# Performance work log

Hardware: AMD Instinct MI355X
Metric: run time of the kernel (lower is better)

Reference implementation:

```python
import jax, jax.numpy as jnp
import numpy as np

N_MLP = 1024  # number of independent tiny MLPs
D_IN, D_HID, D_OUT = 2, 4, 1
B = 16384


def setup_inputs() -> dict:
    key = jax.random.key(0)
    k = jax.random.split(key, 6)
    x = jax.random.normal(k[0], (B, N_MLP), dtype=jnp.float32)
    x_aug = jax.random.normal(k[1], (B, N_MLP), dtype=jnp.float32)
    # Stacked per-MLP parameters (nn.Linear default init ~ U(-1/sqrt(fan_in), 1/sqrt(fan_in)))
    s1 = 1.0 / np.sqrt(D_IN)
    s2 = 1.0 / np.sqrt(D_HID)
    W1 = jax.random.uniform(k[2], (N_MLP, D_HID, D_IN), jnp.float32, -s1, s1)
    b1 = jax.random.uniform(k[3], (N_MLP, D_HID), jnp.float32, -s1, s1)
    W2 = jax.random.uniform(k[4], (N_MLP, D_OUT, D_HID), jnp.float32, -s2, s2)
    b2 = jax.random.uniform(k[5], (N_MLP, D_OUT), jnp.float32, -s2, s2)
    return {"x": x, "x_aug": x_aug, "W1": W1, "b1": b1, "W2": W2, "b2": b2}


def reference(x, x_aug, W1, b1, W2, b2):
    # data: [B, N, 2] — pair (original, augmented) per feature
    data = jnp.stack([x, x_aug], axis=-1)
    # batched tiny GEMM across the N_MLP axis: [B,N,2] x [N,4,2] -> [B,N,4]
    h = jax.nn.relu(jnp.einsum('bne,nhe->bnh', data, W1) + b1)
    # [B,N,4] x [N,1,4] -> [B,N,1]
    o = jnp.einsum('bnh,noh->bno', h, W2) + b2
    # concat over dim1 of per-MLP [B,1] outputs == squeeze -> [B,N]; mean over N -> [B]
    return jnp.mean(o[..., 0], axis=1)
```

## Files before the change

kernel.cpp:

```cpp
#include <hip/hip_runtime.h>


constexpr int N_MLP = 1024;
constexpr int BATCH = 16384;
constexpr int ROWS = 16;
constexpr int NTHREADS = 256;
constexpr int QN = 256;
constexpr int NQ = N_MLP / QN;

typedef __attribute__((address_space(3))) void lds_void;
typedef const __attribute__((address_space(1))) void gbl_void;

__global__ __launch_bounds__(256)
void zero_out_kernel(float* __restrict__ out) {
    out[blockIdx.x * 256 + threadIdx.x] = 0.0f;
}

__global__ __launch_bounds__(NTHREADS)
void disc_mlp_kernel(const float* __restrict__ x,
                     const float* __restrict__ xa,
                     const float* __restrict__ W1,
                     const float* __restrict__ b1,
                     const float* __restrict__ W2,
                     const float* __restrict__ b2,
                     float* __restrict__ out)
{
    __shared__ float xbuf[ROWS * QN];
    __shared__ float abuf[ROWS * QN];
    __shared__ float red[NTHREADS / 64][ROWS];

    const int t    = threadIdx.x;
    const int lane = t & 63;
    const int wave = t >> 6;
    const int q  = blockIdx.x & (NQ - 1);
    const int rb = blockIdx.x >> 2;
    const int b0 = rb * ROWS;
    const int n  = q * QN + t;

    const float4 p0 = reinterpret_cast<const float4*>(W1)[(size_t)n * 2];
    const float4 p1 = reinterpret_cast<const float4*>(W1)[(size_t)n * 2 + 1];
    const float4 bb = reinterpret_cast<const float4*>(b1)[n];
    const float4 ww = reinterpret_cast<const float4*>(W2)[n];
    const float  b2r = b2[n];

    const float* gx = x  + (size_t)b0 * N_MLP + q * QN;
    const float* ga = xa + (size_t)b0 * N_MLP + q * QN;
#pragma unroll
    for (int i = 0; i < ROWS / 4; ++i) {
        const int r = wave * (ROWS / 4) + i;
        const float* srcx = gx + (size_t)r * N_MLP + lane * 4;
        const float* srca = ga + (size_t)r * N_MLP + lane * 4;
        __builtin_amdgcn_global_load_lds((gbl_void*)srcx,
                                         (lds_void*)&xbuf[r * QN + lane * 4],
                                         16, 0, 0);
        __builtin_amdgcn_global_load_lds((gbl_void*)srca,
                                         (lds_void*)&abuf[r * QN + lane * 4],
                                         16, 0, 0);
    }
    __syncthreads();

    const float A[4]   = {p0.x, p0.z, p1.x, p1.z};
    const float C[4]   = {p0.y, p0.w, p1.y, p1.w};
    const float B1r[4] = {bb.x, bb.y, bb.z, bb.w};
    const float V[4]   = {ww.x, ww.y, ww.z, ww.w};

    float acc[ROWS];
#pragma unroll
    for (int r = 0; r < ROWS; ++r) {
        const float xe  = xbuf[r * QN + t];
        const float xae = abuf[r * QN + t];
        float s = b2r;
#pragma unroll
        for (int j = 0; j < 4; ++j) {
            float h = fmaf(A[j], xe, fmaf(C[j], xae, B1r[j]));
            h = fmaxf(h, 0.0f);
            s = fmaf(V[j], h, s);
        }
        acc[r] = s;
    }

#pragma unroll
    for (int r = 0; r < ROWS; ++r) {
        float v = acc[r];
        v += __shfl_down(v, 32);
        v += __shfl_down(v, 16);
        v += __shfl_down(v, 8);
        v += __shfl_down(v, 4);
        v += __shfl_down(v, 2);
        v += __shfl_down(v, 1);
        if (lane == 0) red[wave][r] = v;
    }
    __syncthreads();
    if (t < ROWS) {
        float s = (red[0][t] + red[1][t]) + (red[2][t] + red[3][t]);
        atomicAdd(out + b0 + t, s * (1.0f / (float)N_MLP));
    }
}

extern "C" void kernel_launch(void* const* d_in, const int* in_sizes, int n_in,
                              void* d_out, int out_size, void* d_ws, size_t ws_size,
                              hipStream_t stream) {
    const float* x  = (const float*)d_in[0];
    const float* xa = (const float*)d_in[1];
    const float* W1 = (const float*)d_in[2];
    const float* b1 = (const float*)d_in[3];
    const float* W2 = (const float*)d_in[4];
    const float* b2 = (const float*)d_in[5];
    float* out = (float*)d_out;

    zero_out_kernel<<<BATCH / 256, 256, 0, stream>>>(out);
    disc_mlp_kernel<<<(BATCH / ROWS) * NQ, NTHREADS, 0, stream>>>(x, xa, W1, b1, W2, b2, out);
}
```

Before: 150.2 us.

## Make blocks persistent with double-buffered LDS prefetch across row chunks

Launches a fixed grid of 512 slots per quarter, each looping over several 8-row chunks and prefetching the next chunk into a second LDS buffer while computing the current one. The cross-wave LDS reduction is dropped in favour of one atomicAdd per wave per row. The goal is to overlap global loads with compute and amortize weight loads, at the cost of more global atomics and less parallelism per launch.

```diff
diff --git a/kernel.cpp b/kernel.cpp
--- a/kernel.cpp
+++ b/kernel.cpp
@@ -3,10 +3,12 @@
 
 constexpr int N_MLP = 1024;
 constexpr int BATCH = 16384;
-constexpr int ROWS = 16;
+constexpr int ROWS = 8;
+constexpr int QN = 256;
+constexpr int NQ = 4;
 constexpr int NTHREADS = 256;
-constexpr int QN = 256;
-constexpr int NQ = N_MLP / QN;
+constexpr int SLOTS = 512;
+constexpr int NCHUNK = (BATCH / ROWS) / SLOTS;
 
 typedef __attribute__((address_space(3))) void lds_void;
 typedef const __attribute__((address_space(1))) void gbl_void;
@@ -25,17 +27,15 @@
                      const float* __restrict__ b2,
                      float* __restrict__ out)
 {
-    __shared__ float xbuf[ROWS * QN];
-    __shared__ float abuf[ROWS * QN];
-    __shared__ float red[NTHREADS / 64][ROWS];
+    __shared__ float xbuf[2][ROWS * QN];
+    __shared__ float abuf[2][ROWS * QN];
 
     const int t    = threadIdx.x;
     const int lane = t & 63;
     const int wave = t >> 6;
-    const int q  = blockIdx.x & (NQ - 1);
-    const int rb = blockIdx.x >> 2;
-    const int b0 = rb * ROWS;
-    const int n  = q * QN + t;
+    const int q    = blockIdx.x & (NQ - 1);
+    const int slot = blockIdx.x >> 2;
+    const int n    = q * QN + t;
 
     const float4 p0 = reinterpret_cast<const float4*>(W1)[(size_t)n * 2];
     const float4 p1 = reinterpret_cast<const float4*>(W1)[(size_t)n * 2 + 1];
@@ -43,57 +43,57 @@
     const float4 ww = reinterpret_cast<const float4*>(W2)[n];
     const float  b2r = b2[n];
 
-    const float* gx = x  + (size_t)b0 * N_MLP + q * QN;
-    const float* ga = xa + (size_t)b0 * N_MLP + q * QN;
+    const float* gx = x  + q * QN;
+    const float* ga = xa + q * QN;
+
+    auto stage = [&](int c, int d) {
 #pragma unroll
-    for (int i = 0; i < ROWS / 4; ++i) {
-        const int r = wave * (ROWS / 4) + i;
-        const float* srcx = gx + (size_t)r * N_MLP + lane * 4;
-        const float* srca = ga + (size_t)r * N_MLP + lane * 4;
-        __builtin_amdgcn_global_load_lds((gbl_void*)srcx,
-                                         (lds_void*)&xbuf[r * QN + lane * 4],
-                                         16, 0, 0);
-        __builtin_amdgcn_global_load_lds((gbl_void*)srca,
-                                         (lds_void*)&abuf[r * QN + lane * 4],
-                                         16, 0, 0);
-    }
-    __syncthreads();
+        for (int i = 0; i < ROWS / 4; ++i) {
+            const int r = wave * (ROWS / 4) + i;
+            const size_t off = ((size_t)(c * ROWS + r)) * N_MLP + lane * 4;
+            __builtin_amdgcn_global_load_lds((gbl_void*)(gx + off),
+                                             (lds_void*)&xbuf[d][r * QN + lane * 4],
+                                             16, 0, 0);
+            __builtin_amdgcn_global_load_lds((gbl_void*)(ga + off),
+                                             (lds_void*)&abuf[d][r * QN + lane * 4],
+                                             16, 0, 0);
+        }
+    };
 
     const float A[4]   = {p0.x, p0.z, p1.x, p1.z};
     const float C[4]   = {p0.y, p0.w, p1.y, p1.w};
     const float B1r[4] = {bb.x, bb.y, bb.z, bb.w};
     const float V[4]   = {ww.x, ww.y, ww.z, ww.w};
 
-    float acc[ROWS];
+    stage(slot, 0);
+    int d = 0;
 #pragma unroll
-    for (int r = 0; r < ROWS; ++r) {
-        const float xe  = xbuf[r * QN + t];
-        const float xae = abuf[r * QN + t];
-        float s = b2r;
+    for (int k = 0; k < NCHUNK; ++k) {
+        const int chunk = slot + k * SLOTS;
+        __syncthreads();
+        if (k + 1 < NCHUNK) stage(slot + (k + 1) * SLOTS, d ^ 1);
+
+        const int b0 = chunk * ROWS;
 #pragma unroll
-        for (int j = 0; j < 4; ++j) {
-            float h = fmaf(A[j], xe, fmaf(C[j], xae, B1r[j]));
-            h = fmaxf(h, 0.0f);
-            s = fmaf(V[j], h, s);
+        for (int r = 0; r < ROWS; ++r) {
+            const float xe  = xbuf[d][r * QN + t];
+            const float xae = abuf[d][r * QN + t];
+            float s = b2r;
+#pragma unroll
+            for (int j = 0; j < 4; ++j) {
+                float h = fmaf(A[j], xe, fmaf(C[j], xae, B1r[j]));
+                h = fmaxf(h, 0.0f);
+                s = fmaf(V[j], h, s);
+            }
+            s += __shfl_down(s, 32);
+            s += __shfl_down(s, 16);
+            s += __shfl_down(s, 8);
+            s += __shfl_down(s, 4);
+            s += __shfl_down(s, 2);
+            s += __shfl_down(s, 1);
+            if (lane == 0) atomicAdd(out + b0 + r, s * (1.0f / (float)N_MLP));
         }
-        acc[r] = s;
-    }
-
-#pragma unroll
-    for (int r = 0; r < ROWS; ++r) {
-        float v = acc[r];
-        v += __shfl_down(v, 32);
-        v += __shfl_down(v, 16);
-        v += __shfl_down(v, 8);
-        v += __shfl_down(v, 4);
-        v += __shfl_down(v, 2);
-        v += __shfl_down(v, 1);
-        if (lane == 0) red[wave][r] = v;
-    }
-    __syncthreads();
-    if (t < ROWS) {
-        float s = (red[0][t] + red[1][t]) + (red[2][t] + red[3][t]);
-        atomicAdd(out + b0 + t, s * (1.0f / (float)N_MLP));
+        d ^= 1;
     }
 }
 
@@ -109,5 +109,5 @@
     float* out = (float*)d_out;
 
     zero_out_kernel<<<BATCH / 256, 256, 0, stream>>>(out);
-    disc_mlp_kernel<<<(BATCH / ROWS) * NQ, NTHREADS, 0, stream>>>(x, xa, W1, b1, W2, b2, out);
+    disc_mlp_kernel<<<SLOTS * NQ, NTHREADS, 0, stream>>>(x, xa, W1, b1, W2, b2, out);
 }
```

Measured after the change: 168.8 us. 12.3% more time.
